# Optimization experiments

Hardware: AMD Instinct MI355X
Metric: run time of the kernel (lower is better)

The kernel has to match this reference:

```python
import jax, jax.numpy as jnp
import numpy as np

N, E, G = 50000, 800000, 64          # nodes, edges, graphs
IN, HID, OUT, H = 256, 64, 64, 4     # input dim, per-head hidden, output dim, heads
NEG_SLOPE = 0.2                      # PyG GATConv leaky_relu slope


def _lin(k, fan_in, fan_out):
    return jax.random.normal(k, (fan_in, fan_out), jnp.float32) * (1.0 / np.sqrt(fan_in))


def setup_inputs() -> dict:
    key = jax.random.key(0)
    ks = jax.random.split(key, 16)
    x = jax.random.normal(ks[0], (N, IN), jnp.float32)
    edge_index = jax.random.randint(ks[1], (2, E), 0, N, dtype=jnp.int32)
    batch = jnp.sort(jax.random.randint(ks[2], (N,), 0, G, dtype=jnp.int32))
    # layer 1: IN -> H x HID (concat)
    W1 = _lin(ks[3], IN, H * HID)
    a_src1 = jax.random.normal(ks[4], (H, HID), jnp.float32) * 0.1
    a_dst1 = jax.random.normal(ks[5], (H, HID), jnp.float32) * 0.1
    b1 = jnp.zeros((H * HID,), jnp.float32)
    # layer 2: H*HID -> H x HID (concat)
    W2 = _lin(ks[6], H * HID, H * HID)
    a_src2 = jax.random.normal(ks[7], (H, HID), jnp.float32) * 0.1
    a_dst2 = jax.random.normal(ks[8], (H, HID), jnp.float32) * 0.1
    b2 = jnp.zeros((H * HID,), jnp.float32)
    W3 = _lin(ks[9], H * HID, OUT)
    a_src3 = jax.random.normal(ks[10], (1, OUT), jnp.float32) * 0.1
    a_dst3 = jax.random.normal(ks[11], (1, OUT), jnp.float32) * 0.1
    b3 = jnp.zeros((OUT,), jnp.float32)
    return {"x": x, "edge_index": edge_index, "batch": batch,
            "W1": W1, "a_src1": a_src1, "a_dst1": a_dst1, "b1": b1,
            "W2": W2, "a_src2": a_src2, "a_dst2": a_dst2, "b2": b2,
            "W3": W3, "a_src3": a_src3, "a_dst3": a_dst3, "b3": b3}


def gat_conv(x, src, dst, W, a_src, a_dst, b, heads, out_ch):
    """PyG-style GATConv (eval mode, concat=True semantics; heads=1 == no concat)."""
    n = x.shape[0]
    h = (x @ W).reshape(n, heads, out_ch)                     # [N,H,C]
    alpha_s = jnp.sum(h * a_src, axis=-1)                     # [N,H]
    alpha_d = jnp.sum(h * a_dst, axis=-1)                     # [N,H]
    e = jax.nn.leaky_relu(alpha_s[src] + alpha_d[dst], NEG_SLOPE)  # [E',H]
    # segment softmax over destination nodes (self-loops guarantee nonempty segments)
    m = jax.ops.segment_max(e, dst, num_segments=n)
    e = jnp.exp(e - m[dst])
    denom = jax.ops.segment_sum(e, dst, num_segments=n)
    alpha = e / (denom[dst] + 1e-16)                          # [E',H]
    msg = h[src] * alpha[:, :, None]                          # [E',H,C]
    out = jax.ops.segment_sum(msg, dst, num_segments=n)       # [N,H,C]
    return out.reshape(n, heads * out_ch) + b


def reference(x, edge_index, batch, W1, a_src1, a_dst1, b1, W2, a_src2, a_dst2, b2,
              W3, a_src3, a_dst3, b3):
    n = x.shape[0]
    # GATConv default add_self_loops=True
    loops = jnp.arange(n, dtype=edge_index.dtype)
    src = jnp.concatenate([edge_index[0], loops])
    dst = jnp.concatenate([edge_index[1], loops])

    h = gat_conv(x, src, dst, W1, a_src1, a_dst1, b1, H, HID)
    h = jax.nn.elu(h)  # dropout disabled in eval
    h = gat_conv(h, src, dst, W2, a_src2, a_dst2, b2, H, HID)
    h = jax.nn.elu(h)
    node_embeddings = gat_conv(h, src, dst, W3, a_src3, a_dst3, b3, 1, OUT)

    # global_mean_pool over batch ids
    sums = jax.ops.segment_sum(node_embeddings, batch, num_segments=G)
    counts = jax.ops.segment_sum(jnp.ones((n,), node_embeddings.dtype), batch, num_segments=G)
    graph_embeddings = sums / jnp.maximum(counts, 1.0)[:, None]
    return node_embeddings, graph_embeddings
```

## Files before the change

kernel.cpp:

```cpp
#include <hip/hip_runtime.h>
#include <hip/hip_bf16.h>
#include <hip/hip_fp16.h>

typedef __attribute__((ext_vector_type(8))) _Float16 f16x8;
typedef __attribute__((ext_vector_type(4))) _Float16 f16x4;
typedef __attribute__((ext_vector_type(4))) float f32x4;

static __device__ __forceinline__ void st(float* p, float v)  { *p = v; }
static __device__ __forceinline__ void st(__half* p, float v) { *p = __float2half(v); }

static __device__ __forceinline__ void splitf16(float v, __half& hi, __half& lo) {
    hi = __float2half(v);
    lo = __float2half(v - __half2float(hi));
}

static __device__ __forceinline__ void gload16(const void* g, void* l) {
    __builtin_amdgcn_global_load_lds(
        (const __attribute__((address_space(1))) unsigned int*)g,
        (__attribute__((address_space(3))) unsigned int*)l, 16, 0, 0);
}

static __device__ __forceinline__ void stage_tile(const __half* __restrict__ src,
                                                  int row0, int kc, int K,
                                                  __half* lds, int wave, int lane) {
#pragma unroll
    for (int i = 0; i < 2; ++i) {
        int chunk = i * 4 + wave;
        int row   = chunk * 16 + (lane >> 2);
        int kseg  = (lane & 3) * 8;
        gload16(src + (size_t)(row0 + row) * K + kc + kseg, lds + chunk * 512);
    }
}

__global__ void k_pre(const int* __restrict__ ei, int* __restrict__ deg, int* __restrict__ rnk,
                      int E,
                      const float* __restrict__ x, __half* __restrict__ xh,
                      __half* __restrict__ xl, long n4,
                      const float* __restrict__ W1, const float* __restrict__ W2,
                      const float* __restrict__ W3,
                      __half* __restrict__ w1h, __half* __restrict__ w1l,
                      __half* __restrict__ w2h, __half* __restrict__ w2l,
                      __half* __restrict__ w3h, __half* __restrict__ w3l) {
    int bx = blockIdx.x;
    int nhist = (E + 255) >> 8;
    if (bx < nhist) {
        int e = bx * 256 + threadIdx.x;
        if (e < E) rnk[e] = atomicAdd(&deg[ei[E + e]], 1);
        return;
    }
    bx -= nhist;
    int nx4 = (int)((n4 + 255) >> 8);
    if (bx < nx4) {
        long i = (long)bx * 256 + threadIdx.x;
        if (i < n4) {
            float4 v = *reinterpret_cast<const float4*>(x + i * 4);
            __half h0, h1, h2, h3, l0, l1, l2, l3;
            splitf16(v.x, h0, l0);
            splitf16(v.y, h1, l1);
            splitf16(v.z, h2, l2);
            splitf16(v.w, h3, l3);
            ushort4 hv = { __half_as_ushort(h0), __half_as_ushort(h1),
                           __half_as_ushort(h2), __half_as_ushort(h3) };
            ushort4 lv = { __half_as_ushort(l0), __half_as_ushort(l1),
                           __half_as_ushort(l2), __half_as_ushort(l3) };
            *reinterpret_cast<ushort4*>(xh + i * 4) = hv;
            *reinterpret_cast<ushort4*>(xl + i * 4) = lv;
        }
        return;
    }
    bx -= nx4;
    int idx = bx * 256 + threadIdx.x;
    const float* W; __half *Wh, *Wl; int M, base;
    constexpr int K = 256;
    if (idx < 65536)       { W = W1; Wh = w1h; Wl = w1l; M = 256; base = idx; }
    else if (idx < 131072) { W = W2; Wh = w2h; Wl = w2l; M = 256; base = idx - 65536; }
    else if (idx < 147456) { W = W3; Wh = w3h; Wl = w3l; M = 64;  base = idx - 131072; }
    else return;
    int k = base / M, n = base - k * M;
    __half h, l;
    splitf16(W[base], h, l);
    Wh[(size_t)n * K + k] = h;
    Wl[(size_t)n * K + k] = l;
}

__global__ void k_scan1(const int* __restrict__ deg, int* __restrict__ offs,
                        int* __restrict__ bsum, int N) {
    __shared__ int sh[256];
    int i = blockIdx.x * 256 + threadIdx.x;
    int v = (i < N) ? (deg[i] + 1) : 0;
    sh[threadIdx.x] = v;
    __syncthreads();
#pragma unroll
    for (int off = 1; off < 256; off <<= 1) {
        int t = (threadIdx.x >= off) ? sh[threadIdx.x - off] : 0;
        __syncthreads();
        sh[threadIdx.x] += t;
        __syncthreads();
    }
    if (i < N) offs[i] = sh[threadIdx.x] - v;
    if (threadIdx.x == 255) bsum[blockIdx.x] = sh[255];
}

__global__ void k_scan2(int* __restrict__ bsum, int nb) {
    __shared__ int sh[256];
    int v = (threadIdx.x < nb) ? bsum[threadIdx.x] : 0;
    sh[threadIdx.x] = v;
    __syncthreads();
#pragma unroll
    for (int off = 1; off < 256; off <<= 1) {
        int t = (threadIdx.x >= off) ? sh[threadIdx.x - off] : 0;
        __syncthreads();
        sh[threadIdx.x] += t;
        __syncthreads();
    }
    if (threadIdx.x < nb) bsum[threadIdx.x] = sh[threadIdx.x] - v;
    if (threadIdx.x == 255) bsum[nb] = sh[255];
}

__global__ void k_scan3(int* __restrict__ offs, const int* __restrict__ deg,
                        int* __restrict__ csr, const int* __restrict__ bsum,
                        int N, int nb) {
    int i = blockIdx.x * 256 + threadIdx.x;
    if (i < N) {
        int v = offs[i] + bsum[blockIdx.x];
        offs[i] = v;
        csr[v + deg[i]] = i;
    }
    if (i == 0) offs[N] = bsum[nb];
}

template <typename ACC>
static __device__ __forceinline__ void alpha_epilogue(
        const ACC& acc, float* ldsf, const float* __restrict__ a_src,
        const float* __restrict__ a_dst, float* __restrict__ als,
        float* __restrict__ ald, __half* __restrict__ C,
        int nrows, int M, int H, int r0, int c0,
        int wr, int wc, int quad, int r, int tid) {
    float ps[4][4], pd[4][4];
#pragma unroll
    for (int tr = 0; tr < 4; ++tr)
#pragma unroll
        for (int i = 0; i < 4; ++i) { ps[tr][i] = 0.f; pd[tr][i] = 0.f; }

#pragma unroll
    for (int tr = 0; tr < 4; ++tr)
#pragma unroll
        for (int tc = 0; tc < 2; ++tc) {
            int col = c0 + wc * 32 + tc * 16 + r;
            float av_s = a_src[col], av_d = a_dst[col];
#pragma unroll
            for (int i = 0; i < 4; ++i) {
                int row = r0 + wr * 64 + tr * 16 + quad * 4 + i;
                __half hv = __float2half(acc[tr][tc][i]);
                float vr = __half2float(hv);
                if (row < nrows) C[(size_t)row * M + col] = hv;
                ps[tr][i] = fmaf(vr, av_s, ps[tr][i]);
                pd[tr][i] = fmaf(vr, av_d, pd[tr][i]);
            }
        }
#pragma unroll
    for (int tr = 0; tr < 4; ++tr)
#pragma unroll
        for (int i = 0; i < 4; ++i) {
            float s = ps[tr][i], d2 = pd[tr][i];
#pragma unroll
            for (int off = 1; off < 16; off <<= 1) {
                s  += __shfl_xor(s,  off, 64);
                d2 += __shfl_xor(d2, off, 64);
            }
            if (r == 0) {
                int lrow = wr * 64 + tr * 16 + quad * 4 + i;
                ldsf[(0 * 2 + wc) * 128 + lrow] = s;
                ldsf[(2 + wc) * 128 + lrow]     = d2;
            }
        }
    __syncthreads();
    int lrow = tid >> 1, which = tid & 1;
    if (lrow < 128) {
        float v = ldsf[(which * 2 + 0) * 128 + lrow] + ldsf[(which * 2 + 1) * 128 + lrow];
        int grow = r0 + lrow;
        if (grow < nrows) {
            float* dst = which ? ald : als;
            dst[(size_t)grow * H + (c0 >> 6)] = v;
        }
    }
}

template <typename ACC>
static __device__ __forceinline__ void alpha_epilogue_w(
        const ACC& acc, const float* __restrict__ a_src, const float* __restrict__ a_dst,
        float* __restrict__ als, float* __restrict__ ald, __half* __restrict__ C,
        int nrows, int M, int H, int r0, int c0, int wr, int wc, int quad, int r) {
    int head = (c0 >> 6) + wc;
    float ps[4][4], pd[4][4];
#pragma unroll
    for (int tr = 0; tr < 4; ++tr)
#pragma unroll
        for (int i = 0; i < 4; ++i) { ps[tr][i] = 0.f; pd[tr][i] = 0.f; }

#pragma unroll
    for (int tr = 0; tr < 4; ++tr)
#pragma unroll
        for (int tc = 0; tc < 4; ++tc) {
            int col = c0 + wc * 64 + tc * 16 + r;
            float av_s = a_src[col], av_d = a_dst[col];
#pragma unroll
            for (int i = 0; i < 4; ++i) {
                int row = r0 + wr * 64 + tr * 16 + quad * 4 + i;
                __half hv = __float2half(acc[tr][tc][i]);
                float vr = __half2float(hv);
                if (row < nrows) C[(size_t)row * M + col] = hv;
                ps[tr][i] = fmaf(vr, av_s, ps[tr][i]);
                pd[tr][i] = fmaf(vr, av_d, pd[tr][i]);
            }
        }
#pragma unroll
    for (int tr = 0; tr < 4; ++tr)
#pragma unroll
        for (int i = 0; i < 4; ++i) {
            float s = ps[tr][i], d2 = pd[tr][i];
#pragma unroll
            for (int off = 1; off < 16; off <<= 1) {
                s  += __shfl_xor(s,  off, 64);
                d2 += __shfl_xor(d2, off, 64);
            }
            if (r == 0) {
                int row = r0 + wr * 64 + tr * 16 + quad * 4 + i;
                if (row < nrows) {
                    als[(size_t)row * H + head] = s;
                    ald[(size_t)row * H + head] = d2;
                }
            }
        }
}

__global__ __launch_bounds__(256) void k_g3s(const __half* __restrict__ Ah, const __half* __restrict__ Al,
                                             const __half* __restrict__ Wth, const __half* __restrict__ Wtl,
                                             __half* __restrict__ C, int nrows, int K, int M,
                                             const float* __restrict__ a_src, const float* __restrict__ a_dst,
                                             float* __restrict__ als, float* __restrict__ ald, int H,
                                             int gridRows,
                                             const int* __restrict__ ei, const int* __restrict__ rnk,
                                             const int* __restrict__ offs, int* __restrict__ csr, int E) {
    constexpr int LDA = 32;
    __shared__ __half AH[128 * LDA];
    __shared__ __half AL[128 * LDA];
    __shared__ __half BH[128 * LDA];
    __shared__ __half BL[128 * LDA];

    int gx = blockIdx.x;
    int g = gx / 5, rsel = gx - g * 5;
    if (rsel != 0) {
        int e = (g * 4 + (rsel - 1)) * 256 + threadIdx.x;
        if (e < E) {
            int dn = ei[E + e];
            csr[offs[dn] + rnk[e]] = ei[e];
        }
        return;
    }
    int bxg = g % gridRows, byg = g / gridRows;

    int tid  = threadIdx.x;
    int lane = tid & 63;
    int wave = tid >> 6;
    int wr = wave & 1, wc = wave >> 1;
    int quad = lane >> 4, r = lane & 15;
    int r0 = bxg * 128, c0 = byg * 128;

    f32x4 acc[4][4];
#pragma unroll
    for (int i = 0; i < 4; ++i)
#pragma unroll
        for (int j = 0; j < 4; ++j) acc[i][j] = (f32x4){0.f, 0.f, 0.f, 0.f};

    for (int kc = 0; kc < K; kc += 32) {
        stage_tile(Ah,  r0, kc, K, AH, wave, lane);
        stage_tile(Al,  r0, kc, K, AL, wave, lane);
        stage_tile(Wth, c0, kc, K, BH, wave, lane);
        stage_tile(Wtl, c0, kc, K, BL, wave, lane);
        __syncthreads();
        int k0 = quad * 8;
        f16x8 ah[4], al[4], bh[4], bl[4];
#pragma unroll
        for (int tr = 0; tr < 4; ++tr) {
            int row = wr * 64 + tr * 16 + r;
            ah[tr] = *reinterpret_cast<const f16x8*>(&AH[row * LDA + k0]);
            al[tr] = *reinterpret_cast<const f16x8*>(&AL[row * LDA + k0]);
        }
#pragma unroll
        for (int tc = 0; tc < 4; ++tc) {
            int col = wc * 64 + tc * 16 + r;
            bh[tc] = *reinterpret_cast<const f16x8*>(&BH[col * LDA + k0]);
            bl[tc] = *reinterpret_cast<const f16x8*>(&BL[col * LDA + k0]);
        }
#pragma unroll
        for (int tr = 0; tr < 4; ++tr)
#pragma unroll
            for (int tc = 0; tc < 4; ++tc) {
                acc[tr][tc] = __builtin_amdgcn_mfma_f32_16x16x32_f16(ah[tr], bh[tc], acc[tr][tc], 0, 0, 0);
                acc[tr][tc] = __builtin_amdgcn_mfma_f32_16x16x32_f16(ah[tr], bl[tc], acc[tr][tc], 0, 0, 0);
                acc[tr][tc] = __builtin_amdgcn_mfma_f32_16x16x32_f16(al[tr], bh[tc], acc[tr][tc], 0, 0, 0);
            }
        __syncthreads();
    }
    alpha_epilogue_w(acc, a_src, a_dst, als, ald, C, nrows, M, H, r0, c0, wr, wc, quad, r);
}

__global__ __launch_bounds__(256) void k_gemm2w(const __half* __restrict__ A,
                                                const __half* __restrict__ Wth, const __half* __restrict__ Wtl,
                                                __half* __restrict__ C, int nrows, int K, int M,
                                                const float* __restrict__ a_src, const float* __restrict__ a_dst,
                                                float* __restrict__ als, float* __restrict__ ald, int H) {
    constexpr int LDA = 32;
    __shared__ __half AS[128 * LDA];
    __shared__ __half BH[128 * LDA];
    __shared__ __half BL[128 * LDA];

    int tid  = threadIdx.x;
    int lane = tid & 63;
    int wave = tid >> 6;
    int wr = wave & 1, wc = wave >> 1;
    int quad = lane >> 4, r = lane & 15;
    int r0 = blockIdx.x * 128, c0 = blockIdx.y * 128;

    f32x4 acc[4][4];
#pragma unroll
    for (int i = 0; i < 4; ++i)
#pragma unroll
        for (int j = 0; j < 4; ++j) acc[i][j] = (f32x4){0.f, 0.f, 0.f, 0.f};

    for (int kc = 0; kc < K; kc += 32) {
        stage_tile(A,   r0, kc, K, AS, wave, lane);
        stage_tile(Wth, c0, kc, K, BH, wave, lane);
        stage_tile(Wtl, c0, kc, K, BL, wave, lane);
        __syncthreads();
        int k0 = quad * 8;
        f16x8 a[4], bh[4], bl[4];
#pragma unroll
        for (int tr = 0; tr < 4; ++tr) {
            int row = wr * 64 + tr * 16 + r;
            a[tr] = *reinterpret_cast<const f16x8*>(&AS[row * LDA + k0]);
        }
#pragma unroll
        for (int tc = 0; tc < 4; ++tc) {
            int col = wc * 64 + tc * 16 + r;
            bh[tc] = *reinterpret_cast<const f16x8*>(&BH[col * LDA + k0]);
            bl[tc] = *reinterpret_cast<const f16x8*>(&BL[col * LDA + k0]);
        }
#pragma unroll
        for (int tr = 0; tr < 4; ++tr)
#pragma unroll
            for (int tc = 0; tc < 4; ++tc) {
                acc[tr][tc] = __builtin_amdgcn_mfma_f32_16x16x32_f16(a[tr], bh[tc], acc[tr][tc], 0, 0, 0);
                acc[tr][tc] = __builtin_amdgcn_mfma_f32_16x16x32_f16(a[tr], bl[tc], acc[tr][tc], 0, 0, 0);
            }
        __syncthreads();
    }
    alpha_epilogue_w(acc, a_src, a_dst, als, ald, C, nrows, M, H, r0, c0, wr, wc, quad, r);
}

__global__ __launch_bounds__(256) void k_gemm2(const __half* __restrict__ A,
                                               const __half* __restrict__ Wth, const __half* __restrict__ Wtl,
                                               __half* __restrict__ C, int nrows, int K, int M,
                                               const float* __restrict__ a_src, const float* __restrict__ a_dst,
                                               float* __restrict__ als, float* __restrict__ ald, int H) {
    constexpr int LDA = 40;
    __shared__ __half AS[128 * LDA];
    __shared__ __half BH[64 * LDA];
    __shared__ __half BL[64 * LDA];

    int tid  = threadIdx.x;
    int lane = tid & 63;
    int wave = tid >> 6;
    int wr = wave & 1, wc = wave >> 1;
    int quad = lane >> 4, r = lane & 15;
    int r0 = blockIdx.x * 128, c0 = blockIdx.y * 64;

    f32x4 acc[4][2];
#pragma unroll
    for (int i = 0; i < 4; ++i)
#pragma unroll
        for (int j = 0; j < 2; ++j) acc[i][j] = (f32x4){0.f, 0.f, 0.f, 0.f};

    for (int kc = 0; kc < K; kc += 32) {
#pragma unroll
        for (int it = 0; it < 2; ++it) {
            int row  = (tid >> 2) + it * 64;
            int kseg = (tid & 3) * 8;
            int gr = r0 + row;
            f16x8 v = (f16x8)(_Float16)0;
            if (gr < nrows) v = *reinterpret_cast<const f16x8*>(A + (size_t)gr * K + kc + kseg);
            *reinterpret_cast<f16x8*>(&AS[row * LDA + kseg]) = v;
        }
        {
            int n    = tid >> 2;
            int kseg = (tid & 3) * 8;
            *reinterpret_cast<f16x8*>(&BH[n * LDA + kseg]) =
                *reinterpret_cast<const f16x8*>(Wth + (size_t)(c0 + n) * K + kc + kseg);
            *reinterpret_cast<f16x8*>(&BL[n * LDA + kseg]) =
                *reinterpret_cast<const f16x8*>(Wtl + (size_t)(c0 + n) * K + kc + kseg);
        }
        __syncthreads();
        int k0 = quad * 8;
        f16x8 a[4], bh[2], bl[2];
#pragma unroll
        for (int tr = 0; tr < 4; ++tr) {
            int row = wr * 64 + tr * 16 + r;
            a[tr] = *reinterpret_cast<const f16x8*>(&AS[row * LDA + k0]);
        }
#pragma unroll
        for (int tc = 0; tc < 2; ++tc) {
            int col = wc * 32 + tc * 16 + r;
            bh[tc] = *reinterpret_cast<const f16x8*>(&BH[col * LDA + k0]);
            bl[tc] = *reinterpret_cast<const f16x8*>(&BL[col * LDA + k0]);
        }
#pragma unroll
        for (int tr = 0; tr < 4; ++tr)
#pragma unroll
            for (int tc = 0; tc < 2; ++tc) {
                acc[tr][tc] = __builtin_amdgcn_mfma_f32_16x16x32_f16(a[tr], bh[tc], acc[tr][tc], 0, 0, 0);
                acc[tr][tc] = __builtin_amdgcn_mfma_f32_16x16x32_f16(a[tr], bl[tc], acc[tr][tc], 0, 0, 0);
            }
        __syncthreads();
    }
    alpha_epilogue(acc, reinterpret_cast<float*>(AS), a_src, a_dst, als, ald, C,
                   nrows, M, H, r0, c0, wr, wc, quad, r, tid);
}

template <int CHUNK, bool ELU, typename OT>
__global__ void k_agg(const __half* __restrict__ feat, const int* __restrict__ offs,
                      const int* __restrict__ csr, const float* __restrict__ als,
                      const float* __restrict__ ald, const float* __restrict__ bias,
                      OT* __restrict__ out, int N) {
    constexpr int M  = 64 * CHUNK;
    constexpr int H  = (CHUNK == 4) ? 4 : 1;
    constexpr int EC = 16;
    constexpr int SH = (CHUNK == 4) ? 9 : 7;

    __shared__ float    shw[4][2][64];
    __shared__ unsigned sho[4][2][EC];

    int tid  = threadIdx.x;
    int lane = tid & 63;
    int wid  = tid >> 6;
    int node = blockIdx.x * 4 + wid;
    if (node >= N) return;

    int ia = lane & 15;
    int ha = (H == 4) ? (lane >> 4) : 0;
    int ho = lane >> 4;

    float adv = ald[(size_t)node * H + ha];

    int beg = offs[node], end = offs[node + 1];
    int d   = end - beg;
    int nc  = (d + EC - 1) >> 4;

    const char* fbase = reinterpret_cast<const char*>(feat) + lane * (CHUNK * 2);

    float acc[CHUNK] = {};
    float den = 0.f;

    int sv = csr[beg + min(ia, min(EC, d) - 1)];
    float xv = als[(size_t)sv * H + ha];
    int sv_n = sv;
    if (nc > 1) {
        int cn = min(EC, d - EC);
        sv_n = csr[beg + EC + min(ia, cn - 1)];
    }

    for (int c = 0; c < nc; ++c) {
        int cnt = min(EC, d - c * EC);

        float e = xv + adv;
        e = (e > 0.f) ? e : 0.2f * e;
        float w = (ia < cnt) ? __expf(e) : 0.f;
        den += w;
        int b = c & 1;
        shw[wid][b][lane] = w;
        if (lane < EC) sho[wid][b][lane] = (unsigned)sv << SH;

        xv = als[(size_t)sv_n * H + ha];
        sv = sv_n;
        if (c + 2 < nc) {
            int cn = min(EC, d - (c + 2) * EC);
            sv_n = csr[beg + (c + 2) * EC + min(ia, cn - 1)];
        }

        const float* wp = &shw[wid][b][ho * EC];
        float4 w0 = *reinterpret_cast<const float4*>(wp);
        float4 w1 = *reinterpret_cast<const float4*>(wp + 4);
        float4 w2 = *reinterpret_cast<const float4*>(wp + 8);
        float4 w3 = *reinterpret_cast<const float4*>(wp + 12);
        const unsigned* op = &sho[wid][b][0];
        uint4 o0 = *reinterpret_cast<const uint4*>(op);
        uint4 o1 = *reinterpret_cast<const uint4*>(op + 4);
        uint4 o2 = *reinterpret_cast<const uint4*>(op + 8);
        uint4 o3 = *reinterpret_cast<const uint4*>(op + 12);
        float    ww[EC] = {w0.x, w0.y, w0.z, w0.w, w1.x, w1.y, w1.z, w1.w,
                           w2.x, w2.y, w2.z, w2.w, w3.x, w3.y, w3.z, w3.w};
        unsigned oo[EC] = {o0.x, o0.y, o0.z, o0.w, o1.x, o1.y, o1.z, o1.w,
                           o2.x, o2.y, o2.z, o2.w, o3.x, o3.y, o3.z, o3.w};
        if constexpr (CHUNK == 4) {
            f16x4 v[EC];
#pragma unroll
            for (int t = 0; t < EC; ++t)
                v[t] = *reinterpret_cast<const f16x4*>(fbase + oo[t]);
#pragma unroll
            for (int t = 0; t < EC; ++t)
#pragma unroll
                for (int j = 0; j < 4; ++j)
                    acc[j] = fmaf((float)v[t][j], ww[t], acc[j]);
        } else {
            __half v[EC];
#pragma unroll
            for (int t = 0; t < EC; ++t)
                v[t] = *reinterpret_cast<const __half*>(fbase + oo[t]);
#pragma unroll
            for (int t = 0; t < EC; ++t)
                acc[0] = fmaf(__half2float(v[t]), ww[t], acc[0]);
        }
    }

#pragma unroll
    for (int off = 1; off < EC; off <<= 1) den += __shfl_xor(den, off, 64);
    float inv = 1.f / (den + 1e-16f);

#pragma unroll
    for (int j = 0; j < CHUNK; ++j) {
        int col = lane * CHUNK + j;
        float v = acc[j] * inv + bias[col];
        if (ELU) v = (v > 0.f) ? v : (__expf(v) - 1.f);
        st(&out[(size_t)node * M + col], v);
    }
}

static __device__ __forceinline__ int lowerb(const int* __restrict__ a, int n, int v) {
    int lo = 0, hi = n;
    while (lo < hi) { int mid = (lo + hi) >> 1; if (a[mid] < v) lo = mid + 1; else hi = mid; }
    return lo;
}

__global__ void k_pool2(const float* __restrict__ ne, const int* __restrict__ batch,
                        float* __restrict__ gout, int N) {
    int g = blockIdx.x;
    int lo = lowerb(batch, N, g);
    int hi = lowerb(batch, N, g + 1);
    int lane = threadIdx.x & 63, row = threadIdx.x >> 6;
    float s = 0.f;
    for (int i = lo + row; i < hi; i += 4) s += ne[(size_t)i * 64 + lane];
    __shared__ float red[4][64];
    red[row][lane] = s;
    __syncthreads();
    if (row == 0) {
        float v = red[0][lane] + red[1][lane] + red[2][lane] + red[3][lane];
        gout[(size_t)g * 64 + lane] = v / fmaxf((float)(hi - lo), 1.f);
    }
}

extern "C" void kernel_launch(void* const* d_in, const int* in_sizes, int n_in,
                              void* d_out, int out_size, void* d_ws, size_t ws_size,
                              hipStream_t stream) {
    const float* x   = (const float*)d_in[0];
    const int* ei    = (const int*)d_in[1];
    const int* batch = (const int*)d_in[2];
    const float* W1  = (const float*)d_in[3];
    const float* as1 = (const float*)d_in[4];
    const float* ad1 = (const float*)d_in[5];
    const float* b1  = (const float*)d_in[6];
    const float* W2  = (const float*)d_in[7];
    const float* as2 = (const float*)d_in[8];
    const float* ad2 = (const float*)d_in[9];
    const float* b2  = (const float*)d_in[10];
    const float* W3  = (const float*)d_in[11];
    const float* as3 = (const float*)d_in[12];
    const float* ad3 = (const float*)d_in[13];
    const float* b3  = (const float*)d_in[14];

    const int N = in_sizes[2];
    const int E = in_sizes[1] / 2;
    const int G = 64;
    float* out = (float*)d_out;

    char* w = (char*)d_ws;
    auto carve = [&](size_t bytes) { char* p = w; w += (bytes + 255) & ~(size_t)255; return p; };
    __half* feat = (__half*)carve((size_t)N * 256 * 2);
    __half* xh   = (__half*)carve((size_t)N * 256 * 2);
    __half* xl   = (__half*)carve((size_t)N * 256 * 2);
    __half* act  = xh;
    float* als   = (float*)carve((size_t)N * 4 * 4);
    float* ald   = (float*)carve((size_t)N * 4 * 4);
    int* deg     = (int*)carve((size_t)N * 4);
    int* offs    = (int*)carve((size_t)(N + 1) * 4);
    int* rnk     = (int*)carve((size_t)E * 4);
    int* csr     = (int*)carve((size_t)(E + N) * 4);
    int nb       = (N + 255) / 256;
    int* bsum    = (int*)carve((size_t)(nb + 1) * 4);
    __half* w1h  = (__half*)carve((size_t)256 * 256 * 2);
    __half* w1l  = (__half*)carve((size_t)256 * 256 * 2);
    __half* w2h  = (__half*)carve((size_t)256 * 256 * 2);
    __half* w2l  = (__half*)carve((size_t)256 * 256 * 2);
    __half* w3h  = (__half*)carve((size_t)256 * 64 * 2);
    __half* w3l  = (__half*)carve((size_t)256 * 64 * 2);

    long n4 = (long)N * 64;
    int nhist = (E + 255) / 256;
    int nx4   = (int)((n4 + 255) / 256);
    int nwspl = (147456 + 255) / 256;

    hipMemsetAsync(deg, 0, (size_t)N * 4, stream);
    k_pre<<<nhist + nx4 + nwspl, 256, 0, stream>>>(ei, deg, rnk, E, x, xh, xl, n4,
                                                   W1, W2, W3, w1h, w1l, w2h, w2l, w3h, w3l);

    k_scan1<<<nb, 256, 0, stream>>>(deg, offs, bsum, N);
    k_scan2<<<1, 256, 0, stream>>>(bsum, nb);
    k_scan3<<<nb, 256, 0, stream>>>(offs, deg, csr, bsum, N, nb);

    int gridRows = (N + 127) / 128;
    int gemmBlocks = gridRows * 2;
    int nodeBlocks = (N + 3) / 4;

    k_g3s<<<5 * gemmBlocks, 256, 0, stream>>>(xh, xl, w1h, w1l, feat, N, 256, 256,
                                              as1, ad1, als, ald, 4,
                                              gridRows, ei, rnk, offs, csr, E);
    k_agg<4, true, __half><<<nodeBlocks, 256, 0, stream>>>(feat, offs, csr, als, ald, b1, act, N);
    k_gemm2w<<<dim3(gridRows, 2), 256, 0, stream>>>(act, w2h, w2l, feat, N, 256, 256,
                                                    as2, ad2, als, ald, 4);
    k_agg<4, true, __half><<<nodeBlocks, 256, 0, stream>>>(feat, offs, csr, als, ald, b2, act, N);
    k_gemm2<<<dim3(gridRows, 1), 256, 0, stream>>>(act, w3h, w3l, feat, N, 256, 64,
                                                   as3, ad3, als, ald, 1);
    k_agg<1, false, float><<<nodeBlocks, 256, 0, stream>>>(feat, offs, csr, als, ald, b3, out, N);

    k_pool2<<<G, 256, 0, stream>>>(out, batch, out + (size_t)N * 64, N);
}
```

Measured before the change: 469.6 us.

## Double-buffer LDS tiles in split-f16 GEMM kernels to overlap loads with MFMA

```diff
diff --git a/kernel.cpp b/kernel.cpp
--- a/kernel.cpp
+++ b/kernel.cpp
@@ -243,10 +243,10 @@
                                              const int* __restrict__ ei, const int* __restrict__ rnk,
                                              const int* __restrict__ offs, int* __restrict__ csr, int E) {
     constexpr int LDA = 32;
-    __shared__ __half AH[128 * LDA];
-    __shared__ __half AL[128 * LDA];
-    __shared__ __half BH[128 * LDA];
-    __shared__ __half BL[128 * LDA];
+    __shared__ __half AH[2][128 * LDA];
+    __shared__ __half AL[2][128 * LDA];
+    __shared__ __half BH[2][128 * LDA];
+    __shared__ __half BL[2][128 * LDA];
 
     int gx = blockIdx.x;
     int g = gx / 5, rsel = gx - g * 5;
@@ -273,25 +273,35 @@
 #pragma unroll
         for (int j = 0; j < 4; ++j) acc[i][j] = (f32x4){0.f, 0.f, 0.f, 0.f};
 
-    for (int kc = 0; kc < K; kc += 32) {
-        stage_tile(Ah,  r0, kc, K, AH, wave, lane);
-        stage_tile(Al,  r0, kc, K, AL, wave, lane);
-        stage_tile(Wth, c0, kc, K, BH, wave, lane);
-        stage_tile(Wtl, c0, kc, K, BL, wave, lane);
-        __syncthreads();
+    int nk = K >> 5;
+    stage_tile(Ah,  r0, 0, K, AH[0], wave, lane);
+    stage_tile(Al,  r0, 0, K, AL[0], wave, lane);
+    stage_tile(Wth, c0, 0, K, BH[0], wave, lane);
+    stage_tile(Wtl, c0, 0, K, BL[0], wave, lane);
+    __syncthreads();
+
+    for (int t = 0; t < nk; ++t) {
+        int cur = t & 1, nxt = cur ^ 1;
+        if (t + 1 < nk) {
+            int kc = (t + 1) << 5;
+            stage_tile(Ah,  r0, kc, K, AH[nxt], wave, lane);
+            stage_tile(Al,  r0, kc, K, AL[nxt], wave, lane);
+            stage_tile(Wth, c0, kc, K, BH[nxt], wave, lane);
+            stage_tile(Wtl, c0, kc, K, BL[nxt], wave, lane);
+        }
         int k0 = quad * 8;
         f16x8 ah[4], al[4], bh[4], bl[4];
 #pragma unroll
         for (int tr = 0; tr < 4; ++tr) {
             int row = wr * 64 + tr * 16 + r;
-            ah[tr] = *reinterpret_cast<const f16x8*>(&AH[row * LDA + k0]);
-            al[tr] = *reinterpret_cast<const f16x8*>(&AL[row * LDA + k0]);
+            ah[tr] = *reinterpret_cast<const f16x8*>(&AH[cur][row * LDA + k0]);
+            al[tr] = *reinterpret_cast<const f16x8*>(&AL[cur][row * LDA + k0]);
         }
 #pragma unroll
         for (int tc = 0; tc < 4; ++tc) {
             int col = wc * 64 + tc * 16 + r;
-            bh[tc] = *reinterpret_cast<const f16x8*>(&BH[col * LDA + k0]);
-            bl[tc] = *reinterpret_cast<const f16x8*>(&BL[col * LDA + k0]);
+            bh[tc] = *reinterpret_cast<const f16x8*>(&BH[cur][col * LDA + k0]);
+            bl[tc] = *reinterpret_cast<const f16x8*>(&BL[cur][col * LDA + k0]);
         }
 #pragma unroll
         for (int tr = 0; tr < 4; ++tr)
@@ -312,9 +322,9 @@
                                                 const float* __restrict__ a_src, const float* __restrict__ a_dst,
                                                 float* __restrict__ als, float* __restrict__ ald, int H) {
     constexpr int LDA = 32;
-    __shared__ __half AS[128 * LDA];
-    __shared__ __half BH[128 * LDA];
-    __shared__ __half BL[128 * LDA];
+    __shared__ __half AS[2][128 * LDA];
+    __shared__ __half BH[2][128 * LDA];
+    __shared__ __half BL[2][128 * LDA];
 
     int tid  = threadIdx.x;
     int lane = tid & 63;
@@ -329,23 +339,32 @@
 #pragma unroll
         for (int j = 0; j < 4; ++j) acc[i][j] = (f32x4){0.f, 0.f, 0.f, 0.f};
 
-    for (int kc = 0; kc < K; kc += 32) {
-        stage_tile(A,   r0, kc, K, AS, wave, lane);
-        stage_tile(Wth, c0, kc, K, BH, wave, lane);
-        stage_tile(Wtl, c0, kc, K, BL, wave, lane);
-        __syncthreads();
+    int nk = K >> 5;
+    stage_tile(A,   r0, 0, K, AS[0], wave, lane);
+    stage_tile(Wth, c0, 0, K, BH[0], wave, lane);
+    stage_tile(Wtl, c0, 0, K, BL[0], wave, lane);
+    __syncthreads();
+
+    for (int t = 0; t < nk; ++t) {
+        int cur = t & 1, nxt = cur ^ 1;
+        if (t + 1 < nk) {
+            int kc = (t + 1) << 5;
+            stage_tile(A,   r0, kc, K, AS[nxt], wave, lane);
+            stage_tile(Wth, c0, kc, K, BH[nxt], wave, lane);
+            stage_tile(Wtl, c0, kc, K, BL[nxt], wave, lane);
+        }
         int k0 = quad * 8;
         f16x8 a[4], bh[4], bl[4];
 #pragma unroll
         for (int tr = 0; tr < 4; ++tr) {
             int row = wr * 64 + tr * 16 + r;
-            a[tr] = *reinterpret_cast<const f16x8*>(&AS[row * LDA + k0]);
+            a[tr] = *reinterpret_cast<const f16x8*>(&AS[cur][row * LDA + k0]);
         }
 #pragma unroll
         for (int tc = 0; tc < 4; ++tc) {
             int col = wc * 64 + tc * 16 + r;
-            bh[tc] = *reinterpret_cast<const f16x8*>(&BH[col * LDA + k0]);
-            bl[tc] = *reinterpret_cast<const f16x8*>(&BL[col * LDA + k0]);
+            bh[tc] = *reinterpret_cast<const f16x8*>(&BH[cur][col * LDA + k0]);
+            bl[tc] = *reinterpret_cast<const f16x8*>(&BL[cur][col * LDA + k0]);
         }
 #pragma unroll
         for (int tr = 0; tr < 4; ++tr)
```

Result: no change. 474.6 us (+1.0%).

## Split GAT aggregation into edge-weight pass and column-sliced gather kernel

Applied to the files above, without the earlier changes.

```diff
diff --git a/kernel.cpp b/kernel.cpp
--- a/kernel.cpp
+++ b/kernel.cpp
@@ -425,6 +425,119 @@
     }
     alpha_epilogue(acc, reinterpret_cast<float*>(AS), a_src, a_dst, als, ald, C,
                    nrows, M, H, r0, c0, wr, wc, quad, r, tid);
+}
+
+__global__ void k_wts(const int* __restrict__ offs, const int* __restrict__ csr,
+                      const float* __restrict__ als, const float* __restrict__ ald,
+                      float* __restrict__ wpl, float* __restrict__ invd, int N, int EN) {
+    constexpr int EC = 16;
+    int tid  = threadIdx.x;
+    int lane = tid & 63;
+    int wid  = tid >> 6;
+    int node = blockIdx.x * 4 + wid;
+    if (node >= N) return;
+    int ia = lane & 15, ha = lane >> 4;
+    float adv = ald[(size_t)node * 4 + ha];
+    int beg = offs[node], end = offs[node + 1];
+    int d   = end - beg;
+    int nc  = (d + EC - 1) >> 4;
+    float den = 0.f;
+
+    int sv = csr[beg + min(ia, min(EC, d) - 1)];
+    float xv = als[(size_t)sv * 4 + ha];
+    int sv_n = sv;
+    if (nc > 1) {
+        int cn = min(EC, d - EC);
+        sv_n = csr[beg + EC + min(ia, cn - 1)];
+    }
+    for (int c = 0; c < nc; ++c) {
+        int cnt = min(EC, d - c * EC);
+        float e = xv + adv;
+        e = (e > 0.f) ? e : 0.2f * e;
+        float w = (ia < cnt) ? __expf(e) : 0.f;
+        den += w;
+        if (ia < cnt) wpl[(size_t)ha * EN + beg + c * EC + ia] = w;
+        xv = als[(size_t)sv_n * 4 + ha];
+        sv = sv_n;
+        if (c + 2 < nc) {
+            int cn = min(EC, d - (c + 2) * EC);
+            sv_n = csr[beg + (c + 2) * EC + min(ia, cn - 1)];
+        }
+    }
+#pragma unroll
+    for (int off = 1; off < EC; off <<= 1) den += __shfl_xor(den, off, 64);
+    if (ia == 0) invd[(size_t)node * 4 + ha] = 1.f / (den + 1e-16f);
+}
+
+template <bool ELU>
+__global__ void k_aggs(const __half* __restrict__ feat, const int* __restrict__ offs,
+                       const int* __restrict__ csr, const float* __restrict__ wpl,
+                       const float* __restrict__ invd, const float* __restrict__ bias,
+                       __half* __restrict__ out, int N, int EN) {
+    constexpr int EC = 16;
+    __shared__ float    shw[4][2][EC];
+    __shared__ unsigned sho[4][2][EC];
+
+    int tid  = threadIdx.x;
+    int lane = tid & 63;
+    int wid  = tid >> 6;
+    int half = lane >> 5;
+    int hl   = lane & 31;
+    int slice = blockIdx.x & 7;
+    int ng    = blockIdx.x >> 3;
+    int node  = ng * 8 + wid * 2 + half;
+    if (node >= N) return;
+
+    int h   = slice >> 1;
+    int col = h * 64 + (slice & 1) * 32 + hl;
+
+    int beg = offs[node];
+    int d   = offs[node + 1] - beg;
+    int nc  = (d + EC - 1) >> 4;
+
+    const float* wp_pl = wpl + (size_t)h * EN;
+    const char*  fbase = reinterpret_cast<const char*>(feat) + col * 2;
+
+    float acc = 0.f;
+
+    for (int c = 0; c < nc; ++c) {
+        int cnt = min(EC, d - c * EC);
+        if (hl < EC) {
+            int base = beg + c * EC;
+            int ii   = min(hl, cnt - 1);
+            int src  = csr[base + ii];
+            float wv = wp_pl[base + ii];
+            if (hl >= cnt) wv = 0.f;
+            shw[wid][half][hl] = wv;
+            sho[wid][half][hl] = (unsigned)src << 9;
+        }
+        const float* wp = shw[wid][half];
+        float4 w0 = *reinterpret_cast<const float4*>(wp);
+        float4 w1 = *reinterpret_cast<const float4*>(wp + 4);
+        float4 w2 = *reinterpret_cast<const float4*>(wp + 8);
+        float4 w3 = *reinterpret_cast<const float4*>(wp + 12);
+        const unsigned* op = sho[wid][half];
+        uint4 o0 = *reinterpret_cast<const uint4*>(op);
+        uint4 o1 = *reinterpret_cast<const uint4*>(op + 4);
+        uint4 o2 = *reinterpret_cast<const uint4*>(op + 8);
+        uint4 o3 = *reinterpret_cast<const uint4*>(op + 12);
+        float    ww[EC] = {w0.x, w0.y, w0.z, w0.w, w1.x, w1.y, w1.z, w1.w,
+                           w2.x, w2.y, w2.z, w2.w, w3.x, w3.y, w3.z, w3.w};
+        unsigned oo[EC] = {o0.x, o0.y, o0.z, o0.w, o1.x, o1.y, o1.z, o1.w,
+                           o2.x, o2.y, o2.z, o2.w, o3.x, o3.y, o3.z, o3.w};
+        __half v[EC];
+#pragma unroll
+        for (int t = 0; t < EC; ++t)
+            v[t] = *reinterpret_cast<const __half*>(fbase + oo[t]);
+#pragma unroll
+        for (int t = 0; t < EC; ++t)
+            acc = fmaf(__half2float(v[t]), ww[t], acc);
+    }
+
+    float inv = invd[(size_t)node * 4 + h];
+    float v = acc * inv + bias[col];
+    if (ELU) v = (v > 0.f) ? v : (__expf(v) - 1.f);
+    out[(size_t)node * 256 + col] = __float2half(v);
 }
 
 template <int CHUNK, bool ELU, typename OT>
@@ -580,6 +693,7 @@
     const int N = in_sizes[2];
     const int E = in_sizes[1] / 2;
     const int G = 64;
+    const int EN = E + N;
     float* out = (float*)d_out;
 
     char* w = (char*)d_ws;
@@ -588,6 +702,8 @@
     __half* xh   = (__half*)carve((size_t)N * 256 * 2);
     __half* xl   = (__half*)carve((size_t)N * 256 * 2);
     __half* act  = xh;
+    float* wpl   = (float*)xl;
+    float* invd  = (float*)((char*)xl + (size_t)4 * EN * sizeof(float));
     float* als   = (float*)carve((size_t)N * 4 * 4);
     float* ald   = (float*)carve((size_t)N * 4 * 4);
     int* deg     = (int*)carve((size_t)N * 4);
@@ -619,14 +735,17 @@
     int gridRows = (N + 127) / 128;
     int gemmBlocks = gridRows * 2;
     int nodeBlocks = (N + 3) / 4;
+    int sliceBlocks = 8 * ((N + 7) / 8);
 
     k_g3s<<<5 * gemmBlocks, 256, 0, stream>>>(xh, xl, w1h, w1l, feat, N, 256, 256,
                                               as1, ad1, als, ald, 4,
                                               gridRows, ei, rnk, offs, csr, E);
-    k_agg<4, true, __half><<<nodeBlocks, 256, 0, stream>>>(feat, offs, csr, als, ald, b1, act, N);
+    k_wts<<<nodeBlocks, 256, 0, stream>>>(offs, csr, als, ald, wpl, invd, N, EN);
+    k_aggs<true><<<sliceBlocks, 256, 0, stream>>>(feat, offs, csr, wpl, invd, b1, act, N, EN);
     k_gemm2w<<<dim3(gridRows, 2), 256, 0, stream>>>(act, w2h, w2l, feat, N, 256, 256,
                                                     as2, ad2, als, ald, 4);
-    k_agg<4, true, __half><<<nodeBlocks, 256, 0, stream>>>(feat, offs, csr, als, ald, b2, act, N);
+    k_wts<<<nodeBlocks, 256, 0, stream>>>(offs, csr, als, ald, wpl, invd, N, EN);
+    k_aggs<true><<<sliceBlocks, 256, 0, stream>>>(feat, offs, csr, wpl, invd, b2, act, N, EN);
     k_gemm2<<<dim3(gridRows, 1), 256, 0, stream>>>(act, w3h, w3l, feat, N, 256, 64,
                                                    as3, ad3, als, ald, 1);
     k_agg<1, false, float><<<nodeBlocks, 256, 0, stream>>>(feat, offs, csr, als, ald, b3, out, N);
```

After: 550.4 us. 17.2% more time.
